# Kernel tuning notes

Hardware: AMD Instinct MI355X
Metric: run time of the kernel (lower is better)

## Reference

```python
import jax, jax.numpy as jnp
import numpy as np

N = 8192
F_IN = 512
H = 512
E = 128
ALPHA = 0.2
NEG = -9e15


def _xavier(key, shape, gain=1.414):
    fan_in, fan_out = shape[0], shape[1]
    bound = gain * np.sqrt(6.0 / (fan_in + fan_out))
    return jax.random.uniform(key, shape, jnp.float32, -bound, bound)


def setup_inputs() -> dict:
    key = jax.random.key(0)
    ks = jax.random.split(key, 9)
    x = jax.random.normal(ks[0], (N, F_IN), jnp.float32)
    u = jax.random.uniform(ks[1], (N, N), jnp.float32)
    adj = jnp.where(u < 0.05, u, 0.0)
    M = jax.random.uniform(ks[2], (N, N), jnp.float32)
    return {
        "x": x, "adj": adj, "M": M,
        "W1": _xavier(ks[3], (F_IN, H)),
        "a_self1": _xavier(ks[4], (H, 1)),
        "a_neigh1": _xavier(ks[5], (H, 1)),
        "W2": _xavier(ks[6], (H, E)),
        "a_self2": _xavier(ks[7], (E, 1)),
        "a_neigh2": _xavier(ks[8], (E, 1)),
    }


def _gat_layer(x, adj, M, W, a_self, a_neigh):
    h = x @ W                                   # (N, out)
    s = h @ a_self                              # (N, 1)
    n = h @ a_neigh                             # (N, 1)
    e = (s + n.T) * M                           # (N, N) broadcast score sum
    e = jnp.where(e > 0, e, ALPHA * e)          # leaky_relu
    masked = jnp.where(adj > 0, e, NEG)
    attn = jax.nn.softmax(masked, axis=1)
    h_prime = attn @ h
    return jax.nn.elu(h_prime)


def reference(x, adj, M, W1, a_self1, a_neigh1, W2, a_self2, a_neigh2):
    h = _gat_layer(x, adj, M, W1, a_self1, a_neigh1)
    h = _gat_layer(h, adj, M, W2, a_self2, a_neigh2)
    z = h / jnp.maximum(jnp.linalg.norm(h, axis=1, keepdims=True), 1e-12)
    A_pred = jax.nn.sigmoid(z @ z.T)
    return (A_pred, z)
```

## Files before the change

kernel.cpp:

```cpp
#include <hip/hip_runtime.h>
#include <math.h>

#define NNODES 8192
#define CAP 1024
#define KSPLIT 4
#define KCHUNK (NNODES / KSPLIT)

typedef __attribute__((ext_vector_type(8))) short bf16x8;
typedef __attribute__((ext_vector_type(4))) float f32x4;
typedef unsigned short ushort_t;

__device__ inline unsigned short f2bf(float x) {
    unsigned u = __builtin_bit_cast(unsigned, x);
    u += 0x7fffu + ((u >> 16) & 1u);
    return (unsigned short)(u >> 16);
}

#define GLOAD_LDS16(g, l)                                                      \
    __builtin_amdgcn_global_load_lds(                                          \
        (const __attribute__((address_space(1))) void*)(g),                    \
        (__attribute__((address_space(3))) void*)(l), 16, 0, 0)

template <int ROWS>
__device__ inline void stage_tile(ushort_t* lds, const ushort_t* g, size_t ld, int tid)
{
#pragma unroll
    for (int c = 0; c < ROWS / 32; ++c) {
        int row = c * 32 + (tid >> 3);
        int lch = (tid & 7) ^ (row & 7);
        GLOAD_LDS16(g + (size_t)row * ld + lch * 8, lds + (size_t)c * 2048 + tid * 8);
    }
}

__device__ inline int swz_off(int row, int kc) {
    return row * 64 + ((kc ^ (row & 7)) * 8);
}

__global__ __launch_bounds__(256) void gemm64(const float* __restrict__ A,
                                              const float* __restrict__ B,
                                              float* __restrict__ C,
                                              int M, int N, int K)
{
    __shared__ float sA[16][68];
    __shared__ float sB[16][68];

    const int tid = threadIdx.x;
    const int tx = tid & 15, ty = tid >> 4;
    const int bm = blockIdx.x * 64, bn = blockIdx.y * 64;

    float acc[4][4] = {};

    for (int k0 = 0; k0 < K; k0 += 16) {
        for (int l = tid; l < 64 * 16; l += 256) {
            int m = l >> 4, k = l & 15;
            sA[k][m] = A[(size_t)(bm + m) * K + k0 + k];
        }
        for (int l = tid; l < 16 * 64; l += 256) {
            int k = l >> 6, n = l & 63;
            sB[k][n] = B[(size_t)(k0 + k) * N + bn + n];
        }
        __syncthreads();
#pragma unroll
        for (int k = 0; k < 16; ++k) {
            float a[4], b[4];
#pragma unroll
            for (int i = 0; i < 4; ++i) a[i] = sA[k][ty * 4 + i];
#pragma unroll
            for (int j = 0; j < 4; ++j) b[j] = sB[k][tx * 4 + j];
#pragma unroll
            for (int i = 0; i < 4; ++i)
#pragma unroll
                for (int j = 0; j < 4; ++j) acc[i][j] += a[i] * b[j];
        }
        __syncthreads();
    }

#pragma unroll
    for (int i = 0; i < 4; ++i) {
        float4 v = make_float4(acc[i][0], acc[i][1], acc[i][2], acc[i][3]);
        *(float4*)&C[(size_t)(bm + ty * 4 + i) * N + bn + tx * 4] = v;
    }
}

template <int D>
__global__ __launch_bounds__(256) void sn_kernel(const float* __restrict__ h,
                                                 const float* __restrict__ a_s,
                                                 const float* __restrict__ a_n,
                                                 float* __restrict__ sv,
                                                 float* __restrict__ nv)
{
    const int row = (blockIdx.x * 256 + threadIdx.x) >> 6;
    const int lane = threadIdx.x & 63;
    if (row >= NNODES) return;
    const float* hr = h + (size_t)row * D;
    float a0 = 0.f, a1 = 0.f;
#pragma unroll
    for (int k = lane; k < D; k += 64) {
        float hv = hr[k];
        a0 += hv * a_s[k];
        a1 += hv * a_n[k];
    }
#pragma unroll
    for (int o = 32; o; o >>= 1) {
        a0 += __shfl_down(a0, o);
        a1 += __shfl_down(a1, o);
    }
    if (lane == 0) { sv[row] = a0; nv[row] = a1; }
}

__global__ __launch_bounds__(256) void sn128_fused(const float* __restrict__ h,
                                                   const float* __restrict__ a_s,
                                                   const float* __restrict__ a_n,
                                                   float* __restrict__ sv,
                                                   float* __restrict__ nv,
                                                   ushort_t* __restrict__ h2b)
{
    const int row = (blockIdx.x * 256 + threadIdx.x) >> 6;
    const int lane = threadIdx.x & 63;
    if (row >= NNODES) return;
    const float* hr = h + (size_t)row * 128;
    float v0 = hr[lane], v1 = hr[lane + 64];
    h2b[(size_t)row * 128 + lane]      = f2bf(v0);
    h2b[(size_t)row * 128 + lane + 64] = f2bf(v1);
    float a0 = v0 * a_s[lane] + v1 * a_s[lane + 64];
    float a1 = v0 * a_n[lane] + v1 * a_n[lane + 64];
#pragma unroll
    for (int o = 32; o; o >>= 1) {
        a0 += __shfl_down(a0, o);
        a1 += __shfl_down(a1, o);
    }
    if (lane == 0) { sv[row] = a0; nv[row] = a1; }
}

__global__ __launch_bounds__(256) void build_cols(const float* __restrict__ adj,
                                                  unsigned short* __restrict__ cols,
                                                  int* __restrict__ nnzs)
{
    const int lane = threadIdx.x & 63;
    const int row = blockIdx.x * 4 + (threadIdx.x >> 6);
    const float4* arow = (const float4*)(adj + (size_t)row * NNODES);
    const size_t base = (size_t)row * CAP;
    const unsigned long long below = (1ull << lane) - 1ull;

    int off = 0;
    for (int c4 = 0; c4 < NNODES / 4; c4 += 64) {
        float4 a = arow[c4 + lane];
#pragma unroll
        for (int e = 0; e < 4; ++e) {
            float ae = (&a.x)[e];
            unsigned long long mask = __ballot(ae > 0.f);
            if (ae > 0.f) {
                int pos = off + __popcll(mask & below);
                if (pos < CAP)
                    cols[base + pos] = (unsigned short)((c4 + lane) * 4 + e);
            }
            off += __popcll(mask);
        }
    }
    if (lane == 0) nnzs[row] = off;
}

__global__ __launch_bounds__(256) void gather_vals(const unsigned short* __restrict__ cols,
                                                   const float* __restrict__ Mm,
                                                   const int* __restrict__ nnzs,
                                                   float* __restrict__ vals)
{
    const int i = blockIdx.x;
    const int nnz = min(nnzs[i], CAP);
    const size_t base = (size_t)i * CAP;
    const size_t rowoff = (size_t)i * NNODES;
    for (int k = threadIdx.x; k < nnz; k += 256)
        vals[base + k] = Mm[rowoff + cols[base + k]];
}

__global__ __launch_bounds__(256) void softmax_dense(const unsigned short* __restrict__ cols,
                                                     const float* __restrict__ vals,
                                                     const int* __restrict__ nnzs,
                                                     const float* __restrict__ sv,
                                                     const float* __restrict__ nv,
                                                     ushort_t* __restrict__ P)
{
    constexpr int NT = 256;
    __shared__ ushort_t drow[NNODES];
    __shared__ unsigned short scol[CAP];
    __shared__ float sp[CAP];
    __shared__ float reds[4];
    __shared__ float fb;

    const int tid = threadIdx.x;
    const int i = blockIdx.x;
    const int nnz = min(nnzs[i], CAP);
    const float si = sv[i];
    const size_t base = (size_t)i * CAP;

#pragma unroll
    for (int k = 0; k < NNODES / 8 / NT; ++k)
        ((uint4*)drow)[k * NT + tid] = (uint4){0u, 0u, 0u, 0u};

    float lmax = -3.0e38f;
    for (int k = tid; k < nnz; k += NT) {
        unsigned short c = cols[base + k];
        float e = (si + nv[c]) * vals[base + k];
        e = e > 0.f ? e : 0.2f * e;
        scol[k] = c;
        sp[k] = e;
        lmax = fmaxf(lmax, e);
    }
#pragma unroll
    for (int o = 32; o; o >>= 1) lmax = fmaxf(lmax, __shfl_down(lmax, o));
    if ((tid & 63) == 0) reds[tid >> 6] = lmax;
    __syncthreads();
    if (tid == 0) fb = fmaxf(fmaxf(reds[0], reds[1]), fmaxf(reds[2], reds[3]));
    __syncthreads();
    const float m = fb;

    float lsum = 0.f;
    for (int k = tid; k < nnz; k += NT) {
        float p = expf(sp[k] - m);
        sp[k] = p;
        lsum += p;
    }
#pragma unroll
    for (int o = 32; o; o >>= 1) lsum += __shfl_down(lsum, o);
    if ((tid & 63) == 0) reds[tid >> 6] = lsum;
    __syncthreads();
    if (tid == 0) fb = reds[0] + reds[1] + reds[2] + reds[3];
    __syncthreads();
    const float inv = 1.0f / fb;

    for (int k = tid; k < nnz; k += NT)
        drow[scol[k]] = f2bf(sp[k] * inv);
    __syncthreads();

    uint4* dst = (uint4*)(P + (size_t)i * NNODES);
#pragma unroll
    for (int k = 0; k < NNODES / 8 / NT; ++k)
        dst[k * NT + tid] = ((const uint4*)drow)[k * NT + tid];
}

__global__ __launch_bounds__(256) void tcast(const float* __restrict__ in,
                                             ushort_t* __restrict__ out,
                                             int R, int C)
{
    __shared__ ushort_t t[64][66];
    const int bi = blockIdx.x;
    const int bj = blockIdx.y;
    const int c = threadIdx.x & 63, r4 = threadIdx.x >> 6;
#pragma unroll
    for (int i = 0; i < 16; ++i) {
        int r = i * 4 + r4;
        t[r][c] = f2bf(in[(size_t)(bi * 64 + r) * C + bj * 64 + c]);
    }
    __syncthreads();
#pragma unroll
    for (int i = 0; i < 16; ++i) {
        int r = i * 4 + r4;
        out[(size_t)(bj * 64 + r) * R + bi * 64 + c] = t[c][r];
    }
}

__global__ __launch_bounds__(256) void cast_bf(const float* __restrict__ in,
                                               ushort_t* __restrict__ out, int n4)
{
    int i = blockIdx.x * 256 + threadIdx.x;
    if (i >= n4) return;
    float4 v = ((const float4*)in)[i];
    ushort_t o[4] = { f2bf(v.x), f2bf(v.y), f2bf(v.z), f2bf(v.w) };
    *(uint2*)&out[(size_t)i * 4] = *(uint2*)o;
}

template <int ELU>
__global__ __launch_bounds__(256) void gemm_mfma(const ushort_t* __restrict__ A,
                                                 const ushort_t* __restrict__ BT,
                                                 float* __restrict__ C,
                                                 int N, int K)
{
    __shared__ __align__(16) ushort_t At[128 * 64];
    __shared__ __align__(16) ushort_t Bt[128 * 64];

    const int tid = threadIdx.x;
    const int wid = tid >> 6, lane = tid & 63;
    const int wr = wid >> 1, wc = wid & 1;
    const int bm = blockIdx.x * 128;
    const int bn = blockIdx.y * 128;

    f32x4 acc[4][4] = {};

    for (int k0 = 0; k0 < K; k0 += 64) {
        stage_tile<128>(At, A + (size_t)bm * K + k0, K, tid);
        stage_tile<128>(Bt, BT + (size_t)bn * K + k0, K, tid);
        __syncthreads();
#pragma unroll
        for (int kk = 0; kk < 2; ++kk) {
            const int kc = kk * 4 + (lane >> 4);
            bf16x8 af[4], bfr[4];
#pragma unroll
            for (int m = 0; m < 4; ++m) {
                int r = wr * 64 + m * 16 + (lane & 15);
                af[m] = *(const bf16x8*)&At[swz_off(r, kc)];
            }
#pragma unroll
            for (int n = 0; n < 4; ++n) {
                int r = wc * 64 + n * 16 + (lane & 15);
                bfr[n] = *(const bf16x8*)&Bt[swz_off(r, kc)];
            }
#pragma unroll
            for (int m = 0; m < 4; ++m)
#pragma unroll
                for (int n = 0; n < 4; ++n)
                    acc[m][n] = __builtin_amdgcn_mfma_f32_16x16x32_bf16(af[m], bfr[n], acc[m][n], 0, 0, 0);
        }
        __syncthreads();
    }

#pragma unroll
    for (int m = 0; m < 4; ++m)
#pragma unroll
        for (int n = 0; n < 4; ++n)
#pragma unroll
            for (int r_ = 0; r_ < 4; ++r_) {
                int row = bm + wr * 64 + m * 16 + (lane >> 4) * 4 + r_;
                int col = bn + wc * 64 + n * 16 + (lane & 15);
                float v = acc[m][n][r_];
                if (ELU) v = v > 0.f ? v : expm1f(v);
                C[(size_t)row * N + col] = v;
            }
}

__global__ __launch_bounds__(256) void gemm_pv_ksplit(const ushort_t* __restrict__ P,
                                                      const ushort_t* __restrict__ hbT,
                                                      float* __restrict__ part)
{
    __shared__ __align__(16) ushort_t At[128 * 64];
    __shared__ __align__(16) ushort_t Bt[128 * 64];

    const int tid = threadIdx.x;
    const int wid = tid >> 6, lane = tid & 63;
    const int wr = wid >> 1, wc = wid & 1;
    const int bm = blockIdx.x * 128;
    const int bn = blockIdx.y * 128;
    const int kz = blockIdx.z;

    f32x4 acc[4][4] = {};

    const int kbeg = kz * KCHUNK, kend = kbeg + KCHUNK;
    for (int k0 = kbeg; k0 < kend; k0 += 64) {
        stage_tile<128>(At, P + (size_t)bm * NNODES + k0, NNODES, tid);
        stage_tile<128>(Bt, hbT + (size_t)bn * NNODES + k0, NNODES, tid);
        __syncthreads();
#pragma unroll
        for (int kk = 0; kk < 2; ++kk) {
            const int kc = kk * 4 + (lane >> 4);
            bf16x8 af[4], bfr[4];
#pragma unroll
            for (int m = 0; m < 4; ++m) {
                int r = wr * 64 + m * 16 + (lane & 15);
                af[m] = *(const bf16x8*)&At[swz_off(r, kc)];
            }
#pragma unroll
            for (int n = 0; n < 4; ++n) {
                int r = wc * 64 + n * 16 + (lane & 15);
                bfr[n] = *(const bf16x8*)&Bt[swz_off(r, kc)];
            }
#pragma unroll
            for (int m = 0; m < 4; ++m)
#pragma unroll
                for (int n = 0; n < 4; ++n)
                    acc[m][n] = __builtin_amdgcn_mfma_f32_16x16x32_bf16(af[m], bfr[n], acc[m][n], 0, 0, 0);
        }
        __syncthreads();
    }

    float* dst = part + (size_t)kz * NNODES * 512;
#pragma unroll
    for (int m = 0; m < 4; ++m)
#pragma unroll
        for (int n = 0; n < 4; ++n)
#pragma unroll
            for (int r_ = 0; r_ < 4; ++r_) {
                int row = bm + wr * 64 + m * 16 + (lane >> 4) * 4 + r_;
                int col = bn + wc * 64 + n * 16 + (lane & 15);
                dst[(size_t)row * 512 + col] = acc[m][n][r_];
            }
}

__global__ __launch_bounds__(256) void reduce_elu(const float* __restrict__ part,
                                                  float* __restrict__ out)
{
    const size_t S = (size_t)NNODES * 512 / 4;
    size_t i = (size_t)blockIdx.x * 256 + threadIdx.x;
    if (i >= S) return;
    const float4* p = (const float4*)part;
    float4 a = p[i], b = p[i + S], c = p[i + 2 * S], d = p[i + 3 * S];
    float4 r;
    r.x = a.x + b.x + c.x + d.x;
    r.y = a.y + b.y + c.y + d.y;
    r.z = a.z + b.z + c.z + d.z;
    r.w = a.w + b.w + c.w + d.w;
    r.x = r.x > 0.f ? r.x : expm1f(r.x);
    r.y = r.y > 0.f ? r.y : expm1f(r.y);
    r.z = r.z > 0.f ? r.z : expm1f(r.z);
    r.w = r.w > 0.f ? r.w : expm1f(r.w);
    ((float4*)out)[i] = r;
}

__global__ __launch_bounds__(256) void apred_mfma(const ushort_t* __restrict__ zb,
                                                  float* __restrict__ out)
{
    const int bx = blockIdx.x, by = blockIdx.y;
    if (bx > by) return;

    __shared__ __align__(16) char smem[4 * 64 * 68 * 4];
    ushort_t* At = (ushort_t*)smem;
    ushort_t* Bt = (ushort_t*)(smem + 16384);

    const int tid = threadIdx.x;
    const int wid = tid >> 6, lane = tid & 63;
    const int wr = wid >> 1, wc = wid & 1;
    const int bm = bx * 128;
    const int bn = by * 128;

    f32x4 acc[4][4] = {};

#pragma unroll
    for (int k0 = 0; k0 < 128; k0 += 64) {
        stage_tile<128>(At, zb + (size_t)bm * 128 + k0, 128, tid);
        stage_tile<128>(Bt, zb + (size_t)bn * 128 + k0, 128, tid);
        __syncthreads();
#pragma unroll
        for (int kk = 0; kk < 2; ++kk) {
            const int kc = kk * 4 + (lane >> 4);
            bf16x8 af[4], bfr[4];
#pragma unroll
            for (int m = 0; m < 4; ++m) {
                int r = wr * 64 + m * 16 + (lane & 15);
                af[m] = *(const bf16x8*)&At[swz_off(r, kc)];
            }
#pragma unroll
            for (int n = 0; n < 4; ++n) {
                int r = wc * 64 + n * 16 + (lane & 15);
                bfr[n] = *(const bf16x8*)&Bt[swz_off(r, kc)];
            }
#pragma unroll
            for (int m = 0; m < 4; ++m)
#pragma unroll
                for (int n = 0; n < 4; ++n)
                    acc[m][n] = __builtin_amdgcn_mfma_f32_16x16x32_bf16(af[m], bfr[n], acc[m][n], 0, 0, 0);
        }
        __syncthreads();
    }

    float* cb = (float*)smem + (size_t)wid * 64 * 68;
#pragma unroll
    for (int m = 0; m < 4; ++m)
#pragma unroll
        for (int n = 0; n < 4; ++n)
#pragma unroll
            for (int r_ = 0; r_ < 4; ++r_) {
                int rl = m * 16 + (lane >> 4) * 4 + r_;
                int cl = n * 16 + (lane & 15);
                float v = acc[m][n][r_];
                cb[rl * 68 + cl] = 1.0f / (1.0f + expf(-v));
            }

    const int rowbase = bm + wr * 64;
    const int colbase = bn + wc * 64;

#pragma unroll
    for (int j = 0; j < 16; ++j) {
        int rl = j * 4 + (lane >> 4);
        int c4 = (lane & 15) * 4;
        float4 v = *(const float4*)&cb[rl * 68 + c4];
        *(float4*)&out[(size_t)(rowbase + rl) * NNODES + colbase + c4] = v;
    }

    if (bx < by) {
#pragma unroll
        for (int j = 0; j < 16; ++j) {
            int rl2 = j * 4 + (lane >> 4);
            int c4 = (lane & 15) * 4;
            float4 v;
            v.x = cb[(c4 + 0) * 68 + rl2];
            v.y = cb[(c4 + 1) * 68 + rl2];
            v.z = cb[(c4 + 2) * 68 + rl2];
            v.w = cb[(c4 + 3) * 68 + rl2];
            *(float4*)&out[(size_t)(colbase + rl2) * NNODES + rowbase + c4] = v;
        }
    }
}

__global__ __launch_bounds__(256) void attn2_csr(const unsigned short* __restrict__ cols,
                                                 const float* __restrict__ vals,
                                                 const int* __restrict__ nnzs,
                                                 const float* __restrict__ sv,
                                                 const float* __restrict__ nv,
                                                 const ushort_t* __restrict__ h2b,
                                                 float* __restrict__ out)
{
    constexpr int NT = 256;
    __shared__ unsigned short scol[CAP];
    __shared__ float sp[CAP];
    __shared__ float reds[4];
    __shared__ float fb;
    __shared__ float2 part[NT];

    const int tid = threadIdx.x;
    const int i = blockIdx.x;
    const int nnz = min(nnzs[i], CAP);
    const float si = sv[i];
    const size_t base = (size_t)i * CAP;

    float lmax = -3.0e38f;
    for (int k = tid; k < nnz; k += NT) {
        unsigned short c = cols[base + k];
        float e = (si + nv[c]) * vals[base + k];
        e = e > 0.f ? e : 0.2f * e;
        scol[k] = c;
        sp[k] = e;
        lmax = fmaxf(lmax, e);
    }
#pragma unroll
    for (int o = 32; o; o >>= 1) lmax = fmaxf(lmax, __shfl_down(lmax, o));
    if ((tid & 63) == 0) reds[tid >> 6] = lmax;
    __syncthreads();
    if (tid == 0) fb = fmaxf(fmaxf(reds[0], reds[1]), fmaxf(reds[2], reds[3]));
    __syncthreads();
    const float m = fb;

    float lsum = 0.f;
    for (int k = tid; k < nnz; k += NT) {
        float p = expf(sp[k] - m);
        sp[k] = p;
        lsum += p;
    }
#pragma unroll
    for (int o = 32; o; o >>= 1) lsum += __shfl_down(lsum, o);
    if ((tid & 63) == 0) reds[tid >> 6] = lsum;
    __syncthreads();
    if (tid == 0) fb = reds[0] + reds[1] + reds[2] + reds[3];
    __syncthreads();
    const float inv = 1.0f / fb;

    const int g = tid >> 6, lane = tid & 63;
    float ax = 0.f, ay = 0.f;
    for (int k = g; k < nnz; k += 4) {
        float pj = sp[k];
        unsigned hv = *(const unsigned*)&h2b[(size_t)scol[k] * 128 + lane * 2];
        ax += pj * __builtin_bit_cast(float, hv << 16);
        ay += pj * __builtin_bit_cast(float, hv & 0xffff0000u);
    }
    part[tid] = make_float2(ax, ay);
    __syncthreads();
    if (tid < 64) {
        float2 r0 = part[tid], r1 = part[tid + 64], r2 = part[tid + 128], r3 = part[tid + 192];
        float vx = (r0.x + r1.x + r2.x + r3.x) * inv;
        float vy = (r0.y + r1.y + r2.y + r3.y) * inv;
        out[(size_t)i * 128 + tid * 2]     = vx > 0.f ? vx : expm1f(vx);
        out[(size_t)i * 128 + tid * 2 + 1] = vy > 0.f ? vy : expm1f(vy);
    }
}

__global__ __launch_bounds__(256) void norm_kernel(const float* __restrict__ h,
                                                   float* __restrict__ z,
                                                   ushort_t* __restrict__ zb)
{
    const int row = (blockIdx.x * 256 + threadIdx.x) >> 6;
    const int lane = threadIdx.x & 63;
    if (row >= NNODES) return;
    const float* hr = h + (size_t)row * 128;
    float v0 = hr[lane], v1 = hr[lane + 64];
    float ss = v0 * v0 + v1 * v1;
#pragma unroll
    for (int o = 32; o; o >>= 1) ss += __shfl_down(ss, o);
    ss = __shfl(ss, 0);
    float invn = 1.0f / fmaxf(sqrtf(ss), 1e-12f);
    float z0 = v0 * invn, z1 = v1 * invn;
    z[(size_t)row * 128 + lane]      = z0;
    z[(size_t)row * 128 + lane + 64] = z1;
    zb[(size_t)row * 128 + lane]      = f2bf(z0);
    zb[(size_t)row * 128 + lane + 64] = f2bf(z1);
}

template <int D>
__global__ __launch_bounds__(256) void attn_kernel(const float* __restrict__ adj,
                                                   const float* __restrict__ Mm,
                                                   const float* __restrict__ sv,
                                                   const float* __restrict__ nv,
                                                   const float* __restrict__ h,
                                                   float* __restrict__ out)
{
    constexpr int NT = 256;
    constexpr int DCAP = 2048;
    __shared__ float pbuf[NNODES];
    __shared__ int   idxb[DCAP];
    __shared__ int   cnts[NT];
    __shared__ float reds[4];
    __shared__ float fbcast;
    __shared__ int   totc;

    const int tid = threadIdx.x;
    const int i = blockIdx.x;
    const size_t rowoff = (size_t)i * NNODES;
    const float si = sv[i];

    float lmax = -3.0e38f;
    for (int j = tid; j < NNODES; j += NT) {
        float a = adj[rowoff + j];
        float val = -9.0e15f;
        if (a > 0.f) {
            float e = (si + nv[j]) * Mm[rowoff + j];
            val = e > 0.f ? e : 0.2f * e;
            lmax = fmaxf(lmax, val);
        }
        pbuf[j] = val;
    }
#pragma unroll
    for (int o = 32; o; o >>= 1) lmax = fmaxf(lmax, __shfl_down(lmax, o));
    if ((tid & 63) == 0) reds[tid >> 6] = lmax;
    __syncthreads();
    if (tid == 0) fbcast = fmaxf(fmaxf(reds[0], reds[1]), fmaxf(reds[2], reds[3]));
    __syncthreads();
    const float m = fbcast;

    float lsum = 0.f;
    int myc = 0;
    for (int j = tid; j < NNODES; j += NT) {
        float v = pbuf[j];
        float p = (v > -8.9e15f) ? expf(v - m) : 0.f;
        pbuf[j] = p;
        lsum += p;
        if (p > 0.f) myc++;
    }
#pragma unroll
    for (int o = 32; o; o >>= 1) lsum += __shfl_down(lsum, o);
    if ((tid & 63) == 0) reds[tid >> 6] = lsum;
    cnts[tid] = myc;
    __syncthreads();
    if (tid == 0) {
        fbcast = reds[0] + reds[1] + reds[2] + reds[3];
        int run = 0;
        for (int t = 0; t < NT; ++t) { int c = cnts[t]; cnts[t] = run; run += c; }
        totc = run;
    }
    __syncthreads();
    const float inv = 1.0f / fbcast;
    const int nnz = totc;

    if (nnz <= DCAP) {
        int off = cnts[tid];
        for (int j = tid; j < NNODES; j += NT)
            if (pbuf[j] > 0.f) idxb[off++] = j;
    }
    __syncthreads();

    if constexpr (D == 512) {
        const int c = tid;
        float acc0 = 0.f, acc1 = 0.f;
        if (nnz <= DCAP) {
#pragma unroll 4
            for (int t = 0; t < nnz; ++t) {
                int j = idxb[t];
                float pj = pbuf[j];
                const float* hr = h + (size_t)j * 512;
                acc0 += pj * hr[c];
                acc1 += pj * hr[c + 256];
            }
        } else {
            for (int j = 0; j < NNODES; ++j) {
                float pj = pbuf[j];
                if (pj > 0.f) {
                    const float* hr = h + (size_t)j * 512;
                    acc0 += pj * hr[c];
                    acc1 += pj * hr[c + 256];
                }
            }
        }
        float r0 = acc0 * inv, r1 = acc1 * inv;
        out[(size_t)i * 512 + c]       = r0 > 0.f ? r0 : expm1f(r0);
        out[(size_t)i * 512 + c + 256] = r1 > 0.f ? r1 : expm1f(r1);
    } else {
        const int half = tid >> 7;
        const int c = tid & 127;
        float acc = 0.f;
        if (nnz <= DCAP) {
#pragma unroll 4
            for (int t = half; t < nnz; t += 2) {
                int j = idxb[t];
                acc += pbuf[j] * h[(size_t)j * 128 + c];
            }
        } else {
            for (int j = half; j < NNODES; j += 2) {
                float pj = pbuf[j];
                if (pj > 0.f) acc += pj * h[(size_t)j * 128 + c];
            }
        }
        __syncthreads();
        pbuf[tid] = acc;
        __syncthreads();
        if (tid < 128) {
            float r = (pbuf[tid] + pbuf[tid + 128]) * inv;
            out[(size_t)i * 128 + tid] = r > 0.f ? r : expm1f(r);
        }
    }
}

__global__ __launch_bounds__(256) void apred_kernel(const float* __restrict__ z,
                                                    float* __restrict__ out)
{
    __shared__ float sA[32][68];
    __shared__ float sB[32][68];

    const int tid = threadIdx.x;
    const int tx = tid & 15, ty = tid >> 4;
    const int bm = blockIdx.x * 64, bn = blockIdx.y * 64;

    float acc[4][4] = {};

    for (int k0 = 0; k0 < 128; k0 += 32) {
        for (int l = tid; l < 64 * 32; l += 256) {
            int r = l >> 5, kk = l & 31;
            sA[kk][r] = z[(size_t)(bm + r) * 128 + k0 + kk];
            sB[kk][r] = z[(size_t)(bn + r) * 128 + k0 + kk];
        }
        __syncthreads();
#pragma unroll
        for (int kk = 0; kk < 32; ++kk) {
            float a[4], b[4];
#pragma unroll
            for (int i = 0; i < 4; ++i) a[i] = sA[kk][ty * 4 + i];
#pragma unroll
            for (int j = 0; j < 4; ++j) b[j] = sB[kk][tx * 4 + j];
#pragma unroll
            for (int i = 0; i < 4; ++i)
#pragma unroll
                for (int j = 0; j < 4; ++j) acc[i][j] += a[i] * b[j];
        }
        __syncthreads();
    }

#pragma unroll
    for (int i = 0; i < 4; ++i) {
        float4 v;
        v.x = 1.0f / (1.0f + expf(-acc[i][0]));
        v.y = 1.0f / (1.0f + expf(-acc[i][1]));
        v.z = 1.0f / (1.0f + expf(-acc[i][2]));
        v.w = 1.0f / (1.0f + expf(-acc[i][3]));
        *(float4*)&out[(size_t)(bm + ty * 4 + i) * NNODES + bn + tx * 4] = v;
    }
}

extern "C" void kernel_launch(void* const* d_in, const int* in_sizes, int n_in,
                              void* d_out, int out_size, void* d_ws, size_t ws_size,
                              hipStream_t stream)
{
    const float* x   = (const float*)d_in[0];
    const float* adj = (const float*)d_in[1];
    const float* Mm  = (const float*)d_in[2];
    const float* W1  = (const float*)d_in[3];
    const float* as1 = (const float*)d_in[4];
    const float* an1 = (const float*)d_in[5];
    const float* W2  = (const float*)d_in[6];
    const float* as2 = (const float*)d_in[7];
    const float* an2 = (const float*)d_in[8];

    float* out   = (float*)d_out;
    float* Apred = out;
    float* z     = out + (size_t)NNODES * NNODES;

    ushort_t* P    = (ushort_t*)Apred;
    ushort_t* hbT  = (ushort_t*)((char*)Apred + (size_t)134217728);
    float*    part = (float*)((char*)Apred + (size_t)142606336);

    float* ws  = (float*)d_ws;
    float* h1  = ws;
    float* h1p = h1 + (size_t)NNODES * 512;
    float* h2p = h1p + (size_t)NNODES * 512;
    float* sv  = h2p + (size_t)NNODES * 128;
    float* nv  = sv + NNODES;
    float* vals = nv + NNODES;
    unsigned short* cols = (unsigned short*)(vals + (size_t)NNODES * CAP);
    int* nnzs = (int*)(cols + (size_t)NNODES * CAP);
    ushort_t* zb  = (ushort_t*)(nnzs + NNODES);
    ushort_t* h2b = zb + (size_t)NNODES * 128;
    ushort_t* xb  = h2b + (size_t)NNODES * 128;
    ushort_t* W1T = xb + (size_t)NNODES * 512;

    const size_t need = (size_t)((char*)(W1T + 512 * 512) - (char*)d_ws);

    if (ws_size >= need) {
        cast_bf<<<dim3(4096), 256, 0, stream>>>(x, xb, NNODES * 512 / 4);
        tcast<<<dim3(8, 8), 256, 0, stream>>>(W1, W1T, 512, 512);
        gemm_mfma<0><<<dim3(64, 4), 256, 0, stream>>>(xb, W1T, h1, 512, 512);
        sn_kernel<512><<<dim3(2048), 256, 0, stream>>>(h1, as1, an1, sv, nv);

        build_cols<<<dim3(2048), 256, 0, stream>>>(adj, cols, nnzs);
        gather_vals<<<dim3(NNODES), 256, 0, stream>>>(cols, Mm, nnzs, vals);
        softmax_dense<<<dim3(NNODES), 256, 0, stream>>>(cols, vals, nnzs, sv, nv, P);

        tcast<<<dim3(128, 8), 256, 0, stream>>>(h1, hbT, NNODES, 512);
        gemm_pv_ksplit<<<dim3(64, 4, KSPLIT), 256, 0, stream>>>(P, hbT, part);
        reduce_elu<<<dim3(NNODES * 512 / 4 / 256), 256, 0, stream>>>(part, h1p);

        gemm64<<<dim3(128, 2), 256, 0, stream>>>(h1p, W2, h1, NNODES, 128, 512);
        sn128_fused<<<dim3(2048), 256, 0, stream>>>(h1, as2, an2, sv, nv, h2b);
        attn2_csr<<<dim3(NNODES), 256, 0, stream>>>(cols, vals, nnzs, sv, nv, h2b, h2p);

        norm_kernel<<<dim3(2048), 256, 0, stream>>>(h2p, z, zb);
        apred_mfma<<<dim3(64, 64), 256, 0, stream>>>(zb, Apred);
    } else {
        gemm64<<<dim3(128, 8), 256, 0, stream>>>(x, W1, h1, NNODES, 512, 512);
        sn_kernel<512><<<dim3(2048), 256, 0, stream>>>(h1, as1, an1, sv, nv);
        attn_kernel<512><<<dim3(NNODES), 256, 0, stream>>>(adj, Mm, sv, nv, h1, h1p);

        gemm64<<<dim3(128, 2), 256, 0, stream>>>(h1p, W2, h1, NNODES, 128, 512);
        sn_kernel<128><<<dim3(2048), 256, 0, stream>>>(h1, as2, an2, sv, nv);
        attn_kernel<128><<<dim3(NNODES), 256, 0, stream>>>(adj, Mm, sv, nv, h1, h2p);

        norm_kernel<<<dim3(2048), 256, 0, stream>>>(h2p, z, zb);
        apred_kernel<<<dim3(128, 128), 256, 0, stream>>>(z, Apred);
    }
}
```

Measured before the change: 556.7 us.

## Double-buffer LDS tiles in split-K PV GEMM with K=32 steps

Rewrites the main loop of the split-K attention-times-values GEMM to use two LDS buffers with a K step of 32. The next tile is prefetched via global_load_lds while MFMAs run on the current one, and the pre-compute barrier is removed. The aim is to hide global load latency behind compute. In exchange, each barrier and load issue now covers half as much work, and the swizzle changes to a 4-way XOR that may bring more LDS bank conflicts.

```diff
diff --git a/kernel.cpp b/kernel.cpp
--- a/kernel.cpp
+++ b/kernel.cpp
@@ -34,6 +34,10 @@
 
 __device__ inline int swz_off(int row, int kc) {
     return row * 64 + ((kc ^ (row & 7)) * 8);
+}
+
+__device__ inline int swz32(int row, int kc) {
+    return row * 32 + ((kc ^ (row & 3)) * 8);
 }
 
 __global__ __launch_bounds__(256) void gemm64(const float* __restrict__ A,
@@ -331,8 +335,8 @@
                                                       const ushort_t* __restrict__ hbT,
                                                       float* __restrict__ part)
 {
-    __shared__ __align__(16) ushort_t At[128 * 64];
-    __shared__ __align__(16) ushort_t Bt[128 * 64];
+    __shared__ __align__(16) ushort_t At[2][128 * 32];
+    __shared__ __align__(16) ushort_t Bt[2][128 * 32];
 
     const int tid = threadIdx.x;
     const int wid = tid >> 6, lane = tid & 63;
@@ -340,36 +344,59 @@
     const int bm = blockIdx.x * 128;
     const int bn = blockIdx.y * 128;
     const int kz = blockIdx.z;
+    const int kbeg = kz * KCHUNK;
+
+    const ushort_t* gA = P + (size_t)bm * NNODES + kbeg;
+    const ushort_t* gB = hbT + (size_t)bn * NNODES + kbeg;
 
     f32x4 acc[4][4] = {};
 
-    const int kbeg = kz * KCHUNK, kend = kbeg + KCHUNK;
-    for (int k0 = kbeg; k0 < kend; k0 += 64) {
-        stage_tile<128>(At, P + (size_t)bm * NNODES + k0, NNODES, tid);
-        stage_tile<128>(Bt, hbT + (size_t)bn * NNODES + k0, NNODES, tid);
-        __syncthreads();
-#pragma unroll
-        for (int kk = 0; kk < 2; ++kk) {
-            const int kc = kk * 4 + (lane >> 4);
-            bf16x8 af[4], bfr[4];
-#pragma unroll
-            for (int m = 0; m < 4; ++m) {
-                int r = wr * 64 + m * 16 + (lane & 15);
-                af[m] = *(const bf16x8*)&At[swz_off(r, kc)];
-            }
-#pragma unroll
-            for (int n = 0; n < 4; ++n) {
-                int r = wc * 64 + n * 16 + (lane & 15);
-                bfr[n] = *(const bf16x8*)&Bt[swz_off(r, kc)];
-            }
-#pragma unroll
-            for (int m = 0; m < 4; ++m)
-#pragma unroll
-                for (int n = 0; n < 4; ++n)
-                    acc[m][n] = __builtin_amdgcn_mfma_f32_16x16x32_bf16(af[m], bfr[n], acc[m][n], 0, 0, 0);
-        }
-        __syncthreads();
-    }
+#define STAGE32(t, b)                                                          \
+    do {                                                                       \
+        _Pragma("unroll")                                                      \
+        for (int c = 0; c < 2; ++c) {                                          \
+            int row = c * 64 + (tid >> 2);                                     \
+            int lch = (tid & 3) ^ (row & 3);                                   \
+            GLOAD_LDS16(gA + (size_t)row * NNODES + (t) * 32 + lch * 8,        \
+                        &At[b][c * 2048 + tid * 8]);                           \
+            GLOAD_LDS16(gB + (size_t)row * NNODES + (t) * 32 + lch * 8,        \
+                        &Bt[b][c * 2048 + tid * 8]);                           \
+        }                                                                      \
+    } while (0)
+
+    constexpr int NSTEP = KCHUNK / 32;
+    int cur = 0;
+
+    STAGE32(0, 0);
+    __syncthreads();
+
+    for (int t = 0; t < NSTEP; ++t) {
+        if (t + 1 < NSTEP) STAGE32(t + 1, cur ^ 1);
+
+        const ushort_t* A_ = At[cur];
+        const ushort_t* B_ = Bt[cur];
+        const int kc = lane >> 4;
+        bf16x8 af[4], bfr[4];
+#pragma unroll
+        for (int m = 0; m < 4; ++m) {
+            int r = wr * 64 + m * 16 + (lane & 15);
+            af[m] = *(const bf16x8*)&A_[swz32(r, kc)];
+        }
+#pragma unroll
+        for (int n = 0; n < 4; ++n) {
+            int r = wc * 64 + n * 16 + (lane & 15);
+            bfr[n] = *(const bf16x8*)&B_[swz32(r, kc)];
+        }
+#pragma unroll
+        for (int m = 0; m < 4; ++m)
+#pragma unroll
+            for (int n = 0; n < 4; ++n)
+                acc[m][n] = __builtin_amdgcn_mfma_f32_16x16x32_bf16(af[m], bfr[n], acc[m][n], 0, 0, 0);
+
+        __syncthreads();
+        cur ^= 1;
+    }
+#undef STAGE32
 
     float* dst = part + (size_t)kz * NNODES * 512;
 #pragma unroll
```

Measured after the change: 565.1 us. Within noise of the previous version (+1.5%).
